# Kernel tuning notes

Hardware: AMD Instinct MI355X
Metric: run time of the kernel (lower is better)

Reference implementation:

```python
import jax, jax.numpy as jnp
import numpy as np

B, S, HS = 2, 2048, 1024
H, KV, DH = 16, 4, 64
G = H // KV          # GQA group size
EPS = 1e-6
SCALE = DH ** -0.5


def rms_norm(x, w, eps=EPS):
    # normalize in fp32 over last dim, then rescale (matches MTPRMSNorm)
    xf = x.astype(jnp.float32)
    var = jnp.mean(xf * xf, axis=-1, keepdims=True)
    return (w * (xf * jax.lax.rsqrt(var + eps))).astype(x.dtype)


def setup_inputs() -> dict:
    key = jax.random.key(0)
    ks = jax.random.split(key, 6)
    return {
        "hidden_states": jax.random.normal(ks[0], (B, S, HS), jnp.float32),
        "attention_mask": jnp.zeros((1, 1, S, S), jnp.float32),
        "wq": jax.random.normal(ks[1], (HS, H * DH), jnp.float32) * 0.02,
        "wk": jax.random.normal(ks[2], (HS, KV * DH), jnp.float32) * 0.02,
        "wv": jax.random.normal(ks[3], (HS, KV * DH), jnp.float32) * 0.02,
        "wo": jax.random.normal(ks[4], (H * DH, HS), jnp.float32) * 0.02,
        "q_norm_w": jnp.ones((DH,), jnp.float32),
        "k_norm_w": jnp.ones((DH,), jnp.float32),
    }


def reference(hidden_states, attention_mask, wq, wk, wv, wo, q_norm_w, k_norm_w):
    b, s, _ = hidden_states.shape
    # projections -> per-head layout; GQA handled by broadcasting (no repeat)
    q = rms_norm((hidden_states @ wq).reshape(b, s, KV, G, DH), q_norm_w)  # [b,s,kv,g,dh]
    k = rms_norm((hidden_states @ wk).reshape(b, s, KV, DH), k_norm_w)     # [b,s,kv,dh]
    v = (hidden_states @ wv).reshape(b, s, KV, DH)                          # [b,s,kv,dh]

    # scores: [b, kv, g, q, k]
    scores = jnp.einsum("bqhgd,bkhd->bhgqk", q, k) * SCALE
    scores = scores + attention_mask[:, :, None]  # mask broadcasts over (kv,g)
    probs = jax.nn.softmax(scores.astype(jnp.float32), axis=-1).astype(q.dtype)

    out = jnp.einsum("bhgqk,bkhd->bqhgd", probs, v)  # [b,s,kv,g,dh]
    out = out.reshape(b, s, H * DH)
    return out @ wo
```

## Files before the change

### kernel.cpp

```cpp
#include <hip/hip_runtime.h>
#include <hip/hip_bf16.h>


typedef __attribute__((ext_vector_type(8))) short short8_t;
typedef __attribute__((ext_vector_type(4))) float f32x4_t;

__device__ __forceinline__ unsigned short f2bf_bits(float x) {
  unsigned int u = __float_as_uint(x);
  unsigned int r = u + 0x7fff + ((u >> 16) & 1);
  return (unsigned short)(r >> 16);
}
__device__ __forceinline__ float bf2f_bits(unsigned short b) {
  return __uint_as_float(((unsigned int)b) << 16);
}
__device__ __forceinline__ unsigned int cvt_pk_bf16(float lo, float hi) {
  unsigned int r;
  asm("v_cvt_pk_bf16_f32 %0, %1, %2" : "=v"(r) : "v"(lo), "v"(hi));
  return r;
}

__device__ __forceinline__ void async16(void* lds, const void* g) {
  __builtin_amdgcn_global_load_lds(
      (const __attribute__((address_space(1))) void*)g,
      (__attribute__((address_space(3))) void*)lds, 16, 0, 0);
}

__global__ __launch_bounds__(256) void convert_f32_bf16(
    const float* __restrict__ in, unsigned short* __restrict__ out, int n) {
  int i = (blockIdx.x * 256 + threadIdx.x) * 4;
  if (i >= n) return;
  float4 v = *(const float4*)(in + i);
  ushort4 o;
  o.x = f2bf_bits(v.x); o.y = f2bf_bits(v.y);
  o.z = f2bf_bits(v.z); o.w = f2bf_bits(v.w);
  *(ushort4*)(out + i) = o;
}

__global__ __launch_bounds__(256) void pack_weights(
    const float* __restrict__ wq, const float* __restrict__ wk,
    const float* __restrict__ wv, const float* __restrict__ wo,
    unsigned short* __restrict__ Wqkvt, unsigned short* __restrict__ Wot) {
  __shared__ unsigned short T[64][72];
  int b = blockIdx.x;
  const float* W; unsigned short* Wt; int Nsrc, n_off, bx, by;
  if (b < 256)      { W = wq; Wt = Wqkvt; Nsrc = 1024; n_off = 0;    bx = b & 15;          by = b >> 4; }
  else if (b < 320) { W = wk; Wt = Wqkvt; Nsrc = 256;  n_off = 1024; bx = (b - 256) & 3;   by = (b - 256) >> 2; }
  else if (b < 384) { W = wv; Wt = Wqkvt; Nsrc = 256;  n_off = 1280; bx = (b - 320) & 3;   by = (b - 320) >> 2; }
  else              { W = wo; Wt = Wot;   Nsrc = 1024; n_off = 0;    bx = (b - 384) & 15;  by = (b - 384) >> 4; }
  const int tn = bx * 64, tk = by * 64;
  for (int e = threadIdx.x; e < 4096; e += 256) {
    int kk = e >> 6, nn = e & 63;
    T[nn][kk] = f2bf_bits(W[(size_t)(tk + kk) * Nsrc + tn + nn]);
  }
  __syncthreads();
  for (int e = threadIdx.x; e < 4096; e += 256) {
    int nn = e >> 6, kk = e & 63;
    Wt[(size_t)(n_off + tn + nn) * 1024 + tk + kk] = T[nn][kk];
  }
}

__global__ __launch_bounds__(256) void transpose_v(
    const unsigned short* __restrict__ qkv, unsigned short* __restrict__ vt) {
  __shared__ unsigned short T[64][72];
  const int tid = threadIdx.x;
  const int st = blockIdx.x * 64, bk = blockIdx.y;
  const int b = bk >> 2, kvh = bk & 3;
  const unsigned short* src = qkv + (size_t)(b * 2048 + st) * 1536 + 1280 + kvh * 64;
  for (int e = tid; e < 4096; e += 256) {
    int s = e >> 6, d = e & 63;
    T[d][s] = src[(size_t)s * 1536 + d];
  }
  __syncthreads();
  unsigned short* dst = vt + (size_t)bk * 64 * 2048 + st;
  for (int e = tid; e < 4096; e += 256) {
    int d = e >> 6, s = e & 63;
    int p = ((s >> 5) << 5) | (((s >> 2) & 3) << 3) | (((s >> 4) & 1) << 2) | (s & 3);
    dst[(size_t)d * 2048 + p] = T[d][s];
  }
}

__global__ __launch_bounds__(256) void mask_flags(
    const float* __restrict__ mask, int* __restrict__ flags, float* __restrict__ tmax) {
  const int tid = threadIdx.x, w = tid >> 6;
  const int bq = blockIdx.y * 64, bk = blockIdx.x * 64;
  bool nz = false;
  float vmax = -INFINITY;
  #pragma unroll
  for (int i = 0; i < 4; ++i) {
    int e = (i * 256 + tid) * 4;
    int r = e >> 6, c = e & 63;
    float4 v = *(const float4*)(mask + (size_t)(bq + r) * 2048 + bk + c);
    nz |= (v.x != 0.f) | (v.y != 0.f) | (v.z != 0.f) | (v.w != 0.f);
    vmax = fmaxf(vmax, fmaxf(fmaxf(v.x, v.y), fmaxf(v.z, v.w)));
  }
  #pragma unroll
  for (int m = 1; m < 64; m <<= 1) vmax = fmaxf(vmax, __shfl_xor(vmax, m, 64));
  unsigned long long anynz = __ballot((int)nz);
  __shared__ float wm[4];
  __shared__ int wf[4];
  if ((tid & 63) == 0) { wm[w] = vmax; wf[w] = (anynz != 0ull); }
  __syncthreads();
  if (tid == 0) {
    int idx = blockIdx.y * gridDim.x + blockIdx.x;
    flags[idx] = wf[0] | wf[1] | wf[2] | wf[3];
    tmax[idx] = fmaxf(fmaxf(wm[0], wm[1]), fmaxf(wm[2], wm[3]));
  }
}

template <bool OUT_BF16, bool QKNORM>
__global__ __launch_bounds__(256) void gemm_bt(
    const unsigned short* __restrict__ A, const unsigned short* __restrict__ Bt,
    void* __restrict__ Cp, int M, int N, int K, int ldc,
    const float* __restrict__ qw, const float* __restrict__ kw) {
  __shared__ unsigned short As[128 * 32];
  __shared__ unsigned short Bs[128 * 32];
  const int tid = threadIdx.x;
  const int w = tid >> 6, l = tid & 63, lr = l & 15, lg = l >> 4;
  const int nwg = gridDim.x * gridDim.y;
  int orig = blockIdx.y * gridDim.x + blockIdx.x;
  int wgid = ((nwg & 7) == 0) ? ((orig & 7) * (nwg >> 3) + (orig >> 3)) : orig;
  const int bm = (wgid / gridDim.x) * 128, bn = (wgid % gridDim.x) * 128;
  const int wrow = (w >> 1) * 64, wcol = (w & 1) * 64;

  f32x4_t acc[4][4] = {};

  for (int k0 = 0; k0 < K; k0 += 32) {
    __syncthreads();
    #pragma unroll
    for (int i = 0; i < 2; ++i) {
      int c = i * 4 + w;
      const unsigned short* ga = A + (size_t)(bm + c * 16 + (l >> 2)) * K + k0 + (l & 3) * 8;
      async16(As + c * 512, ga);
      const unsigned short* gb = Bt + (size_t)(bn + c * 16 + (l >> 2)) * K + k0 + (l & 3) * 8;
      async16(Bs + c * 512, gb);
    }
    __syncthreads();
    short8_t af[4], bfr[4];
    #pragma unroll
    for (int m = 0; m < 4; ++m)
      af[m] = *(const short8_t*)(As + (wrow + m * 16 + lr) * 32 + lg * 8);
    #pragma unroll
    for (int n = 0; n < 4; ++n)
      bfr[n] = *(const short8_t*)(Bs + (wcol + n * 16 + lr) * 32 + lg * 8);
    #pragma unroll
    for (int m = 0; m < 4; ++m)
      #pragma unroll
      for (int n = 0; n < 4; ++n)
        acc[m][n] = __builtin_amdgcn_mfma_f32_16x16x32_bf16(af[m], bfr[n], acc[m][n], 0, 0, 0);
  }

  if constexpr (QKNORM) {
    int seg = (bn + wcol) >> 6;
    if (seg < 20) {
      const float* wseg = (seg < 16) ? qw : kw;
      float wv[4];
      #pragma unroll
      for (int n = 0; n < 4; ++n) {
        wv[n] = wseg[n * 16 + lr];
        if (seg < 16) wv[n] *= 0.125f;
      }
      #pragma unroll
      for (int m = 0; m < 4; ++m)
        #pragma unroll
        for (int j = 0; j < 4; ++j) {
          float ss = acc[m][0][j] * acc[m][0][j];
          #pragma unroll
          for (int n = 1; n < 4; ++n) ss += acc[m][n][j] * acc[m][n][j];
          #pragma unroll
          for (int x = 1; x < 16; x <<= 1) ss += __shfl_xor(ss, x, 64);
          float rinv = rsqrtf(ss * (1.0f / 64.0f) + 1e-6f);
          #pragma unroll
          for (int n = 0; n < 4; ++n) acc[m][n][j] *= rinv * wv[n];
        }
    }
  }

  #pragma unroll
  for (int m = 0; m < 4; ++m)
    #pragma unroll
    for (int n = 0; n < 4; ++n)
      #pragma unroll
      for (int j = 0; j < 4; ++j) {
        int row = bm + wrow + m * 16 + lg * 4 + j;
        int col = bn + wcol + n * 16 + lr;
        float v = acc[m][n][j];
        if (OUT_BF16) ((unsigned short*)Cp)[(size_t)row * ldc + col] = f2bf_bits(v);
        else          ((float*)Cp)[(size_t)row * ldc + col] = v;
      }
}

__global__ __launch_bounds__(256, 4) void flash_attn(
    const unsigned short* __restrict__ qkv, const unsigned short* __restrict__ vtg,
    const float* __restrict__ mask, const int* __restrict__ flags,
    const float* __restrict__ tmax, const float* __restrict__ qw,
    const float* __restrict__ kw, unsigned short* __restrict__ O) {
  int orig = blockIdx.y * 32 + blockIdx.x;
  int swz = (orig & 7) * 128 + (orig >> 3);
  const int qt = swz & 31, bh = swz >> 5;
  const int b = bh >> 4, hq = bh & 15, kvh = hq >> 2;
  const int tid = threadIdx.x, w = tid >> 6, l = tid & 63, lr = l & 15, lg = l >> 4;

  __shared__ unsigned short Ks[2][64 * 64];
  __shared__ unsigned short Vs[2][64 * 64];

  const unsigned short* Qg = qkv + (size_t)(b * 2048 + qt * 64) * 1536 + hq * 64;
  const unsigned short* Kg = qkv + (size_t)(b * 2048) * 1536 + 1024 + kvh * 64;
  const unsigned short* Vg = vtg + (size_t)(b * 4 + kvh) * 64 * 2048;
  const float* Mg = mask + (size_t)(qt * 64) * 2048;
  const int* Fp = flags + qt * 32;

  auto stage = [&](int kt2, int bi) {
    #pragma unroll
    for (int it = 0; it < 2; ++it) {
      int c = it * 256 + tid;
      int r = c >> 3, cc = (c & 7) ^ (r & 7);
      async16(&Ks[bi][it * 2048 + w * 512],
              Kg + (size_t)(kt2 * 64 + r) * 1536 + cc * 8);
      async16(&Vs[bi][it * 2048 + w * 512],
              Vg + (size_t)r * 2048 + kt2 * 64 + cc * 8);
    }
  };

  stage(0, 0);

  const float L2E = 1.44269504f;
  float pmax = fabsf(qw[l] * kw[l]);
  #pragma unroll
  for (int m = 1; m < 64; m <<= 1) pmax = fmaxf(pmax, __shfl_xor(pmax, m, 64));
  float tmx = (l < 32) ? tmax[qt * 32 + l] : -INFINITY;
  #pragma unroll
  for (int m = 1; m < 64; m <<= 1) tmx = fmaxf(tmx, __shfl_xor(tmx, m, 64));
  const float nm = -(8.0f * pmax + fmaxf(tmx, 0.0f)) * L2E;

  short8_t qf[2];
  {
    const unsigned short* qrow = Qg + (size_t)(w * 16 + lr) * 1536 + lg * 8;
    qf[0] = *(const short8_t*)(qrow);
    qf[1] = *(const short8_t*)(qrow + 32);
  }

  short8_t vb1;
  #pragma unroll
  for (int e = 0; e < 8; ++e) vb1[e] = (lr == 0) ? (short)0x3f80 : (short)0;

  f32x4_t oacc[5] = {};

  for (int kt = 0; kt < 32; ++kt) {
    __syncthreads();
    if (kt < 31) stage(kt + 1, (kt + 1) & 1);
    const int cur = kt & 1;

    f32x4_t sacc[4] = {};
    __builtin_amdgcn_s_setprio(1);
    #pragma unroll
    for (int kd = 0; kd < 2; ++kd)
      #pragma unroll
      for (int n = 0; n < 4; ++n) {
        int kr = n * 16 + lr;
        short8_t kf = *(const short8_t*)(&Ks[cur][kr * 64 + ((kd * 4 + lg) ^ (kr & 7)) * 8]);
        sacc[n] = __builtin_amdgcn_mfma_f32_16x16x32_bf16(kf, qf[kd], sacc[n], 0, 0, 0);
      }
    __builtin_amdgcn_s_setprio(0);

    const bool hasmask = Fp[kt] != 0;
    float e4[4][4];
    #pragma unroll
    for (int n = 0; n < 4; ++n) {
      if (hasmask) {
        float4 mv = *(const float4*)(Mg + (size_t)(w * 16 + lr) * 2048 + kt * 64 + n * 16 + lg * 4);
        e4[n][0] = exp2f(fmaf(sacc[n][0] + mv.x, L2E, nm));
        e4[n][1] = exp2f(fmaf(sacc[n][1] + mv.y, L2E, nm));
        e4[n][2] = exp2f(fmaf(sacc[n][2] + mv.z, L2E, nm));
        e4[n][3] = exp2f(fmaf(sacc[n][3] + mv.w, L2E, nm));
      } else {
        #pragma unroll
        for (int j = 0; j < 4; ++j)
          e4[n][j] = exp2f(fmaf(sacc[n][j], L2E, nm));
      }
    }
    short8_t pa[2];
    #pragma unroll
    for (int kd = 0; kd < 2; ++kd) {
      int4 pk;
      pk.x = (int)cvt_pk_bf16(e4[2 * kd][0],     e4[2 * kd][1]);
      pk.y = (int)cvt_pk_bf16(e4[2 * kd][2],     e4[2 * kd][3]);
      pk.z = (int)cvt_pk_bf16(e4[2 * kd + 1][0], e4[2 * kd + 1][1]);
      pk.w = (int)cvt_pk_bf16(e4[2 * kd + 1][2], e4[2 * kd + 1][3]);
      pa[kd] = *(short8_t*)&pk;
    }

    __builtin_amdgcn_s_setprio(1);
    #pragma unroll
    for (int kd = 0; kd < 2; ++kd) {
      #pragma unroll
      for (int nd = 0; nd < 4; ++nd) {
        int vr = nd * 16 + lr;
        short8_t vb = *(const short8_t*)(&Vs[cur][vr * 64 + ((kd * 4 + lg) ^ (vr & 7)) * 8]);
        oacc[nd] = __builtin_amdgcn_mfma_f32_16x16x32_bf16(pa[kd], vb, oacc[nd], 0, 0, 0);
      }
      oacc[4] = __builtin_amdgcn_mfma_f32_16x16x32_bf16(pa[kd], vb1, oacc[4], 0, 0, 0);
    }
    __builtin_amdgcn_s_setprio(0);
  }

  float rln[4];
  #pragma unroll
  for (int j = 0; j < 4; ++j) rln[j] = 1.0f / __shfl(oacc[4][j], l & 48, 64);
  #pragma unroll
  for (int nd = 0; nd < 4; ++nd)
    #pragma unroll
    for (int j = 0; j < 4; ++j) {
      size_t row = (size_t)(b * 2048 + qt * 64 + w * 16 + lg * 4 + j);
      O[row * 1024 + hq * 64 + nd * 16 + lr] = f2bf_bits(oacc[nd][j] * rln[j]);
    }
}

extern "C" void kernel_launch(void* const* d_in, const int* in_sizes, int n_in,
                              void* d_out, int out_size, void* d_ws, size_t ws_size,
                              hipStream_t stream) {
  const float* hidden = (const float*)d_in[0];
  const float* mask   = (const float*)d_in[1];
  const float* wq     = (const float*)d_in[2];
  const float* wk     = (const float*)d_in[3];
  const float* wv     = (const float*)d_in[4];
  const float* wo     = (const float*)d_in[5];
  const float* qw     = (const float*)d_in[6];
  const float* kw     = (const float*)d_in[7];

  char* ws = (char*)d_ws;
  unsigned short* Xbf   = (unsigned short*)(ws);
  unsigned short* Wqkvt = (unsigned short*)(ws +  8388608);
  unsigned short* Wot   = (unsigned short*)(ws + 11534336);
  unsigned short* QKV   = (unsigned short*)(ws + 13631488);
  unsigned short* Vtg   = Wqkvt;
  int*            flags = (int*)(ws + 10485760);
  float*          tmaxb = (float*)(ws + 10489856);
  unsigned short* Obf   = Xbf;

  convert_f32_bf16<<<4096, 256, 0, stream>>>(hidden, Xbf, 4096 * 1024);
  pack_weights<<<640, 256, 0, stream>>>(wq, wk, wv, wo, Wqkvt, Wot);

  gemm_bt<true, true><<<dim3(12, 32), 256, 0, stream>>>(
      Xbf, Wqkvt, QKV, 4096, 1536, 1024, 1536, qw, kw);
  transpose_v<<<dim3(32, 8), 256, 0, stream>>>(QKV, Vtg);
  mask_flags<<<dim3(32, 32), 256, 0, stream>>>(mask, flags, tmaxb);
  flash_attn<<<dim3(32, 32), 256, 0, stream>>>(QKV, Vtg, mask, flags, tmaxb, qw, kw, Obf);
  gemm_bt<false, false><<<dim3(8, 32), 256, 0, stream>>>(
      Obf, Wot, d_out, 4096, 1024, 1024, 1024, nullptr, nullptr);
}
```

Baseline: 139.8 us.

## Switch attention to 32x32 MFMA with split-K waves and fuse prep kernels

Flash attention now uses 32x32x16 bf16 MFMA. Each pair of waves covers 32 query rows and splits each key tile in half, and the partial outputs and row sums are merged through LDS at the end. The launch bound occupancy hint is dropped. The activation convert, weight pack and mask-scan kernels are merged into one prep launch, with mask flags stored in the tail of the output buffer, which the final GEMM later overwrites. The V permutation is recomputed for the new MFMA operand layout. The goal is fewer launches and fewer LDS fragment reads per MFMA, at the cost of higher register pressure and an extra LDS reduction step.

```diff
diff --git a/kernel.cpp b/kernel.cpp
--- a/kernel.cpp
+++ b/kernel.cpp
@@ -2,8 +2,9 @@
 #include <hip/hip_bf16.h>
 
 
-typedef __attribute__((ext_vector_type(8))) short short8_t;
-typedef __attribute__((ext_vector_type(4))) float f32x4_t;
+typedef __attribute__((ext_vector_type(8)))  short short8_t;
+typedef __attribute__((ext_vector_type(4)))  float f32x4_t;
+typedef __attribute__((ext_vector_type(16))) float f32x16_t;
 
 __device__ __forceinline__ unsigned short f2bf_bits(float x) {
   unsigned int u = __float_as_uint(x);
@@ -25,37 +26,69 @@
       (__attribute__((address_space(3))) void*)lds, 16, 0, 0);
 }
 
-__global__ __launch_bounds__(256) void convert_f32_bf16(
-    const float* __restrict__ in, unsigned short* __restrict__ out, int n) {
-  int i = (blockIdx.x * 256 + threadIdx.x) * 4;
-  if (i >= n) return;
-  float4 v = *(const float4*)(in + i);
-  ushort4 o;
-  o.x = f2bf_bits(v.x); o.y = f2bf_bits(v.y);
-  o.z = f2bf_bits(v.z); o.w = f2bf_bits(v.w);
-  *(ushort4*)(out + i) = o;
-}
-
-__global__ __launch_bounds__(256) void pack_weights(
+__global__ __launch_bounds__(256) void prep(
+    const float* __restrict__ hidden, unsigned short* __restrict__ Xbf,
     const float* __restrict__ wq, const float* __restrict__ wk,
     const float* __restrict__ wv, const float* __restrict__ wo,
-    unsigned short* __restrict__ Wqkvt, unsigned short* __restrict__ Wot) {
+    unsigned short* __restrict__ Wqkvt, unsigned short* __restrict__ Wot,
+    const float* __restrict__ mask, int* __restrict__ flags, float* __restrict__ tmax) {
   __shared__ unsigned short T[64][72];
-  int b = blockIdx.x;
-  const float* W; unsigned short* Wt; int Nsrc, n_off, bx, by;
-  if (b < 256)      { W = wq; Wt = Wqkvt; Nsrc = 1024; n_off = 0;    bx = b & 15;          by = b >> 4; }
-  else if (b < 320) { W = wk; Wt = Wqkvt; Nsrc = 256;  n_off = 1024; bx = (b - 256) & 3;   by = (b - 256) >> 2; }
-  else if (b < 384) { W = wv; Wt = Wqkvt; Nsrc = 256;  n_off = 1280; bx = (b - 320) & 3;   by = (b - 320) >> 2; }
-  else              { W = wo; Wt = Wot;   Nsrc = 1024; n_off = 0;    bx = (b - 384) & 15;  by = (b - 384) >> 4; }
-  const int tn = bx * 64, tk = by * 64;
-  for (int e = threadIdx.x; e < 4096; e += 256) {
-    int kk = e >> 6, nn = e & 63;
-    T[nn][kk] = f2bf_bits(W[(size_t)(tk + kk) * Nsrc + tn + nn]);
-  }
-  __syncthreads();
-  for (int e = threadIdx.x; e < 4096; e += 256) {
-    int nn = e >> 6, kk = e & 63;
-    Wt[(size_t)(n_off + tn + nn) * 1024 + tk + kk] = T[nn][kk];
+  const int tid = threadIdx.x;
+  int blk = blockIdx.x;
+  if (blk < 4096) {
+    int i = (blk * 256 + tid) * 4;
+    float4 v = *(const float4*)(hidden + i);
+    ushort4 o;
+    o.x = f2bf_bits(v.x); o.y = f2bf_bits(v.y);
+    o.z = f2bf_bits(v.z); o.w = f2bf_bits(v.w);
+    *(ushort4*)(Xbf + i) = o;
+    return;
+  }
+  if (blk < 4736) {
+    int b = blk - 4096;
+    const float* W; unsigned short* Wt; int Nsrc, n_off, bx, by;
+    if (b < 256)      { W = wq; Wt = Wqkvt; Nsrc = 1024; n_off = 0;    bx = b & 15;         by = b >> 4; }
+    else if (b < 320) { W = wk; Wt = Wqkvt; Nsrc = 256;  n_off = 1024; bx = (b - 256) & 3;  by = (b - 256) >> 2; }
+    else if (b < 384) { W = wv; Wt = Wqkvt; Nsrc = 256;  n_off = 1280; bx = (b - 320) & 3;  by = (b - 320) >> 2; }
+    else              { W = wo; Wt = Wot;   Nsrc = 1024; n_off = 0;    bx = (b - 384) & 15; by = (b - 384) >> 4; }
+    const int tn = bx * 64, tk = by * 64;
+    for (int e = tid; e < 4096; e += 256) {
+      int kk = e >> 6, nn = e & 63;
+      T[nn][kk] = f2bf_bits(W[(size_t)(tk + kk) * Nsrc + tn + nn]);
+    }
+    __syncthreads();
+    for (int e = tid; e < 4096; e += 256) {
+      int nn = e >> 6, kk = e & 63;
+      Wt[(size_t)(n_off + tn + nn) * 1024 + tk + kk] = T[nn][kk];
+    }
+    return;
+  }
+  {
+    int mb = blk - 4736;
+    const int bx = mb & 31, by = mb >> 5;
+    const int bq = by * 64, bk = bx * 64, w = tid >> 6;
+    bool nz = false;
+    float vmax = -INFINITY;
+    #pragma unroll
+    for (int i = 0; i < 4; ++i) {
+      int e = (i * 256 + tid) * 4;
+      int r = e >> 6, c = e & 63;
+      float4 v = *(const float4*)(mask + (size_t)(bq + r) * 2048 + bk + c);
+      nz |= (v.x != 0.f) | (v.y != 0.f) | (v.z != 0.f) | (v.w != 0.f);
+      vmax = fmaxf(vmax, fmaxf(fmaxf(v.x, v.y), fmaxf(v.z, v.w)));
+    }
+    #pragma unroll
+    for (int m = 1; m < 64; m <<= 1) vmax = fmaxf(vmax, __shfl_xor(vmax, m, 64));
+    unsigned long long anynz = __ballot((int)nz);
+    __shared__ float wm[4];
+    __shared__ int wf[4];
+    if ((tid & 63) == 0) { wm[w] = vmax; wf[w] = (anynz != 0ull); }
+    __syncthreads();
+    if (tid == 0) {
+      int idx = by * 32 + bx;
+      flags[idx] = wf[0] | wf[1] | wf[2] | wf[3];
+      tmax[idx] = fmaxf(fmaxf(wm[0], wm[1]), fmaxf(wm[2], wm[3]));
+    }
   }
 }
 
@@ -74,36 +107,8 @@
   unsigned short* dst = vt + (size_t)bk * 64 * 2048 + st;
   for (int e = tid; e < 4096; e += 256) {
     int d = e >> 6, s = e & 63;
-    int p = ((s >> 5) << 5) | (((s >> 2) & 3) << 3) | (((s >> 4) & 1) << 2) | (s & 3);
+    int p = (s & ~12) | ((s & 4) << 1) | ((s & 8) >> 1);
     dst[(size_t)d * 2048 + p] = T[d][s];
-  }
-}
-
-__global__ __launch_bounds__(256) void mask_flags(
-    const float* __restrict__ mask, int* __restrict__ flags, float* __restrict__ tmax) {
-  const int tid = threadIdx.x, w = tid >> 6;
-  const int bq = blockIdx.y * 64, bk = blockIdx.x * 64;
-  bool nz = false;
-  float vmax = -INFINITY;
-  #pragma unroll
-  for (int i = 0; i < 4; ++i) {
-    int e = (i * 256 + tid) * 4;
-    int r = e >> 6, c = e & 63;
-    float4 v = *(const float4*)(mask + (size_t)(bq + r) * 2048 + bk + c);
-    nz |= (v.x != 0.f) | (v.y != 0.f) | (v.z != 0.f) | (v.w != 0.f);
-    vmax = fmaxf(vmax, fmaxf(fmaxf(v.x, v.y), fmaxf(v.z, v.w)));
-  }
-  #pragma unroll
-  for (int m = 1; m < 64; m <<= 1) vmax = fmaxf(vmax, __shfl_xor(vmax, m, 64));
-  unsigned long long anynz = __ballot((int)nz);
-  __shared__ float wm[4];
-  __shared__ int wf[4];
-  if ((tid & 63) == 0) { wm[w] = vmax; wf[w] = (anynz != 0ull); }
-  __syncthreads();
-  if (tid == 0) {
-    int idx = blockIdx.y * gridDim.x + blockIdx.x;
-    flags[idx] = wf[0] | wf[1] | wf[2] | wf[3];
-    tmax[idx] = fmaxf(fmaxf(wm[0], wm[1]), fmaxf(wm[2], wm[3]));
   }
 }
 
@@ -189,7 +194,7 @@
       }
 }
 
-__global__ __launch_bounds__(256, 4) void flash_attn(
+__global__ __launch_bounds__(256) void flash_attn(
     const unsigned short* __restrict__ qkv, const unsigned short* __restrict__ vtg,
     const float* __restrict__ mask, const int* __restrict__ flags,
     const float* __restrict__ tmax, const float* __restrict__ qw,
@@ -198,10 +203,12 @@
   int swz = (orig & 7) * 128 + (orig >> 3);
   const int qt = swz & 31, bh = swz >> 5;
   const int b = bh >> 4, hq = bh & 15, kvh = hq >> 2;
-  const int tid = threadIdx.x, w = tid >> 6, l = tid & 63, lr = l & 15, lg = l >> 4;
-
-  __shared__ unsigned short Ks[2][64 * 64];
-  __shared__ unsigned short Vs[2][64 * 64];
+  const int tid = threadIdx.x, w = tid >> 6, l = tid & 63;
+  const int qcol = l & 31, h = l >> 5;
+  const int qb = w & 1, kh = w >> 1;
+
+  __shared__ unsigned short SMEM[2][2][64 * 64];
+  float* fb = (float*)SMEM;
 
   const unsigned short* Qg = qkv + (size_t)(b * 2048 + qt * 64) * 1536 + hq * 64;
   const unsigned short* Kg = qkv + (size_t)(b * 2048) * 1536 + 1024 + kvh * 64;
@@ -214,9 +221,9 @@
     for (int it = 0; it < 2; ++it) {
       int c = it * 256 + tid;
       int r = c >> 3, cc = (c & 7) ^ (r & 7);
-      async16(&Ks[bi][it * 2048 + w * 512],
+      async16(&SMEM[0][bi][it * 2048 + w * 512],
               Kg + (size_t)(kt2 * 64 + r) * 1536 + cc * 8);
-      async16(&Vs[bi][it * 2048 + w * 512],
+      async16(&SMEM[1][bi][it * 2048 + w * 512],
               Vg + (size_t)r * 2048 + kt2 * 64 + cc * 8);
     }
   };
@@ -232,87 +239,110 @@
   for (int m = 1; m < 64; m <<= 1) tmx = fmaxf(tmx, __shfl_xor(tmx, m, 64));
   const float nm = -(8.0f * pmax + fmaxf(tmx, 0.0f)) * L2E;
 
-  short8_t qf[2];
-  {
-    const unsigned short* qrow = Qg + (size_t)(w * 16 + lr) * 1536 + lg * 8;
-    qf[0] = *(const short8_t*)(qrow);
-    qf[1] = *(const short8_t*)(qrow + 32);
-  }
+  short8_t qf[4];
+  #pragma unroll
+  for (int s = 0; s < 4; ++s)
+    qf[s] = *(const short8_t*)(Qg + (size_t)(qb * 32 + qcol) * 1536 + s * 16 + h * 8);
 
   short8_t vb1;
   #pragma unroll
-  for (int e = 0; e < 8; ++e) vb1[e] = (lr == 0) ? (short)0x3f80 : (short)0;
-
-  f32x4_t oacc[5] = {};
+  for (int e = 0; e < 8; ++e) vb1[e] = (qcol == 0) ? (short)0x3f80 : (short)0;
+
+  f32x16_t oacc0 = (f32x16_t)0.0f;
+  f32x16_t oacc1 = (f32x16_t)0.0f;
+  f32x16_t osum  = (f32x16_t)0.0f;
 
   for (int kt = 0; kt < 32; ++kt) {
     __syncthreads();
     if (kt < 31) stage(kt + 1, (kt + 1) & 1);
     const int cur = kt & 1;
 
-    f32x4_t sacc[4] = {};
+    f32x16_t sacc = (f32x16_t)0.0f;
     __builtin_amdgcn_s_setprio(1);
     #pragma unroll
-    for (int kd = 0; kd < 2; ++kd)
-      #pragma unroll
-      for (int n = 0; n < 4; ++n) {
-        int kr = n * 16 + lr;
-        short8_t kf = *(const short8_t*)(&Ks[cur][kr * 64 + ((kd * 4 + lg) ^ (kr & 7)) * 8]);
-        sacc[n] = __builtin_amdgcn_mfma_f32_16x16x32_bf16(kf, qf[kd], sacc[n], 0, 0, 0);
-      }
+    for (int s = 0; s < 4; ++s) {
+      int r = kh * 32 + qcol;
+      int cc = (s * 2 + h) ^ (r & 7);
+      short8_t kf = *(const short8_t*)(&SMEM[0][cur][r * 64 + cc * 8]);
+      sacc = __builtin_amdgcn_mfma_f32_32x32x16_bf16(kf, qf[s], sacc, 0, 0, 0);
+    }
     __builtin_amdgcn_s_setprio(0);
 
     const bool hasmask = Fp[kt] != 0;
-    float e4[4][4];
-    #pragma unroll
-    for (int n = 0; n < 4; ++n) {
-      if (hasmask) {
-        float4 mv = *(const float4*)(Mg + (size_t)(w * 16 + lr) * 2048 + kt * 64 + n * 16 + lg * 4);
-        e4[n][0] = exp2f(fmaf(sacc[n][0] + mv.x, L2E, nm));
-        e4[n][1] = exp2f(fmaf(sacc[n][1] + mv.y, L2E, nm));
-        e4[n][2] = exp2f(fmaf(sacc[n][2] + mv.z, L2E, nm));
-        e4[n][3] = exp2f(fmaf(sacc[n][3] + mv.w, L2E, nm));
-      } else {
-        #pragma unroll
-        for (int j = 0; j < 4; ++j)
-          e4[n][j] = exp2f(fmaf(sacc[n][j], L2E, nm));
-      }
-    }
+    float e[16];
+    if (hasmask) {
+      const float* mrow = Mg + (size_t)(qb * 32 + qcol) * 2048 + kt * 64 + kh * 32 + 4 * h;
+      #pragma unroll
+      for (int g = 0; g < 4; ++g) {
+        float4 mv = *(const float4*)(mrow + g * 8);
+        e[g * 4 + 0] = exp2f(fmaf(sacc[g * 4 + 0] + mv.x, L2E, nm));
+        e[g * 4 + 1] = exp2f(fmaf(sacc[g * 4 + 1] + mv.y, L2E, nm));
+        e[g * 4 + 2] = exp2f(fmaf(sacc[g * 4 + 2] + mv.z, L2E, nm));
+        e[g * 4 + 3] = exp2f(fmaf(sacc[g * 4 + 3] + mv.w, L2E, nm));
+      }
+    } else {
+      #pragma unroll
+      for (int r = 0; r < 16; ++r)
+        e[r] = exp2f(fmaf(sacc[r], L2E, nm));
+    }
+    unsigned int u[8];
+    #pragma unroll
+    for (int i = 0; i < 8; ++i) u[i] = cvt_pk_bf16(e[2 * i], e[2 * i + 1]);
     short8_t pa[2];
     #pragma unroll
-    for (int kd = 0; kd < 2; ++kd) {
-      int4 pk;
-      pk.x = (int)cvt_pk_bf16(e4[2 * kd][0],     e4[2 * kd][1]);
-      pk.y = (int)cvt_pk_bf16(e4[2 * kd][2],     e4[2 * kd][3]);
-      pk.z = (int)cvt_pk_bf16(e4[2 * kd + 1][0], e4[2 * kd + 1][1]);
-      pk.w = (int)cvt_pk_bf16(e4[2 * kd + 1][2], e4[2 * kd + 1][3]);
-      pa[kd] = *(short8_t*)&pk;
+    for (int s = 0; s < 2; ++s) {
+      int4 pk = make_int4((int)u[4 * s], (int)u[4 * s + 1], (int)u[4 * s + 2], (int)u[4 * s + 3]);
+      pa[s] = *(short8_t*)&pk;
     }
 
     __builtin_amdgcn_s_setprio(1);
     #pragma unroll
-    for (int kd = 0; kd < 2; ++kd) {
-      #pragma unroll
-      for (int nd = 0; nd < 4; ++nd) {
-        int vr = nd * 16 + lr;
-        short8_t vb = *(const short8_t*)(&Vs[cur][vr * 64 + ((kd * 4 + lg) ^ (vr & 7)) * 8]);
-        oacc[nd] = __builtin_amdgcn_mfma_f32_16x16x32_bf16(pa[kd], vb, oacc[nd], 0, 0, 0);
-      }
-      oacc[4] = __builtin_amdgcn_mfma_f32_16x16x32_bf16(pa[kd], vb1, oacc[4], 0, 0, 0);
+    for (int s = 0; s < 2; ++s) {
+      {
+        int rv = qcol;
+        int cc = (kh * 4 + s * 2 + h) ^ (rv & 7);
+        short8_t vb = *(const short8_t*)(&SMEM[1][cur][rv * 64 + cc * 8]);
+        oacc0 = __builtin_amdgcn_mfma_f32_32x32x16_bf16(pa[s], vb, oacc0, 0, 0, 0);
+      }
+      {
+        int rv = 32 + qcol;
+        int cc = (kh * 4 + s * 2 + h) ^ (rv & 7);
+        short8_t vb = *(const short8_t*)(&SMEM[1][cur][rv * 64 + cc * 8]);
+        oacc1 = __builtin_amdgcn_mfma_f32_32x32x16_bf16(pa[s], vb, oacc1, 0, 0, 0);
+      }
+      osum = __builtin_amdgcn_mfma_f32_32x32x16_bf16(pa[s], vb1, osum, 0, 0, 0);
     }
     __builtin_amdgcn_s_setprio(0);
   }
 
-  float rln[4];
-  #pragma unroll
-  for (int j = 0; j < 4; ++j) rln[j] = 1.0f / __shfl(oacc[4][j], l & 48, 64);
-  #pragma unroll
-  for (int nd = 0; nd < 4; ++nd)
-    #pragma unroll
-    for (int j = 0; j < 4; ++j) {
-      size_t row = (size_t)(b * 2048 + qt * 64 + w * 16 + lg * 4 + j);
-      O[row * 1024 + hq * 64 + nd * 16 + lr] = f2bf_bits(oacc[nd][j] * rln[j]);
-    }
+  __syncthreads();
+  if (kh == 1) {
+    float* fw = fb + (w - 2) * 3072;
+    #pragma unroll
+    for (int r = 0; r < 16; ++r) fw[r * 64 + l]        = oacc0[r];
+    #pragma unroll
+    for (int r = 0; r < 16; ++r) fw[(16 + r) * 64 + l] = oacc1[r];
+    #pragma unroll
+    for (int r = 0; r < 16; ++r) fw[(32 + r) * 64 + l] = osum[r];
+  }
+  __syncthreads();
+  if (kh == 0) {
+    float* fw = fb + w * 3072;
+    #pragma unroll
+    for (int r = 0; r < 16; ++r) oacc0[r] += fw[r * 64 + l];
+    #pragma unroll
+    for (int r = 0; r < 16; ++r) oacc1[r] += fw[(16 + r) * 64 + l];
+    #pragma unroll
+    for (int r = 0; r < 16; ++r) osum[r]  += fw[(32 + r) * 64 + l];
+    #pragma unroll
+    for (int r = 0; r < 16; ++r) {
+      float rln = 1.0f / __shfl(osum[r], l & 32, 64);
+      int qrow = (r & 3) + 8 * (r >> 2) + 4 * h;
+      size_t row = (size_t)(b * 2048 + qt * 64 + qb * 32 + qrow);
+      O[row * 1024 + hq * 64 + qcol]      = f2bf_bits(oacc0[r] * rln);
+      O[row * 1024 + hq * 64 + 32 + qcol] = f2bf_bits(oacc1[r] * rln);
+    }
+  }
 }
 
 extern "C" void kernel_launch(void* const* d_in, const int* in_sizes, int n_in,
@@ -333,17 +363,17 @@
   unsigned short* Wot   = (unsigned short*)(ws + 11534336);
   unsigned short* QKV   = (unsigned short*)(ws + 13631488);
   unsigned short* Vtg   = Wqkvt;
-  int*            flags = (int*)(ws + 10485760);
-  float*          tmaxb = (float*)(ws + 10489856);
   unsigned short* Obf   = Xbf;
 
-  convert_f32_bf16<<<4096, 256, 0, stream>>>(hidden, Xbf, 4096 * 1024);
-  pack_weights<<<640, 256, 0, stream>>>(wq, wk, wv, wo, Wqkvt, Wot);
+  char* dtail = (char*)d_out + (size_t)out_size * 4 - 8192;
+  int*   flags = (int*)dtail;
+  float* tmaxb = (float*)(dtail + 4096);
+
+  prep<<<5760, 256, 0, stream>>>(hidden, Xbf, wq, wk, wv, wo, Wqkvt, Wot, mask, flags, tmaxb);
 
   gemm_bt<true, true><<<dim3(12, 32), 256, 0, stream>>>(
       Xbf, Wqkvt, QKV, 4096, 1536, 1024, 1536, qw, kw);
   transpose_v<<<dim3(32, 8), 256, 0, stream>>>(QKV, Vtg);
-  mask_flags<<<dim3(32, 32), 256, 0, stream>>>(mask, flags, tmaxb);
   flash_attn<<<dim3(32, 32), 256, 0, stream>>>(QKV, Vtg, mask, flags, tmaxb, qw, kw, Obf);
   gemm_bt<false, false><<<dim3(8, 32), 256, 0, stream>>>(
       Obf, Wot, d_out, 4096, 1024, 1024, 1024, nullptr, nullptr);
```

New measurement: 150.3 us. +7.5%, slower.
